# Optimization experiments

Measured on AMD Instinct MI355X. Metric: run time of the kernel, lower is better.

## Reference

```python
import jax, jax.numpy as jnp
import numpy as np

NUM_HEADS = 16


def setup_inputs() -> dict:
    key = jax.random.key(0)
    ks = jax.random.split(key, 8)
    B, S, E = 2, 2048, 1024
    std = 0.02
    return {
        "q": jax.random.normal(ks[0], (B, S, E), dtype=jnp.float32),
        "k": jax.random.normal(ks[1], (B, S, E), dtype=jnp.float32),
        "v": jax.random.normal(ks[2], (B, S, E), dtype=jnp.float32),
        "Wq": jax.random.normal(ks[3], (E, E), dtype=jnp.float32) * std,
        "Wk": jax.random.normal(ks[4], (E, E), dtype=jnp.float32) * std,
        "Wv": jax.random.normal(ks[5], (E, E), dtype=jnp.float32) * std,
        "Wo": jax.random.normal(ks[6], (E, E), dtype=jnp.float32) * std,
        "bo": jnp.zeros((E,), dtype=jnp.float32),
    }


def reference(q, k, v, Wq, Wk, Wv, Wo, bo):
    B, S, E = q.shape
    H = NUM_HEADS
    D = E // H
    # projections (nn.Linear: x @ W.T)
    Q = (q @ Wq.T).reshape(B, S, H, D).transpose(0, 2, 1, 3)  # [B,H,S,D]
    K = (k @ Wk.T).reshape(B, S, H, D).transpose(0, 2, 1, 3)
    V = (v @ Wv.T).reshape(B, S, H, D).transpose(0, 2, 1, 3)
    scores = jnp.einsum("bhsd,bhtd->bhst", Q, K)  # [B,H,S,S]
    # causal mask applied before scaling (as in source; -inf/sqrt(d) == -inf)
    causal = jnp.tril(jnp.ones((S, S), dtype=bool))
    scores = jnp.where(causal, scores, -jnp.inf)
    scores = scores / np.sqrt(D).astype(np.float32)
    attn = jax.nn.softmax(scores, axis=-1)
    out = jnp.einsum("bhst,bhtd->bhsd", attn, V)  # [B,H,S,D]
    out = out.transpose(0, 2, 1, 3).reshape(B, S, E)
    return out @ Wo.T + bo
```

## Files before the change

### kernel.cpp

```cpp
#include <hip/hip_runtime.h>

typedef unsigned short u16;
typedef __bf16 bf16x8 __attribute__((ext_vector_type(8)));
typedef float f32x4 __attribute__((ext_vector_type(4)));
typedef unsigned u32x4 __attribute__((ext_vector_type(4)));

#define B_ 2
#define S_ 2048
#define E_ 1024
#define H_ 16
#define D_ 64
#define M_ (B_ * S_)

__device__ inline u16 f2bf(float f) {
  union { float f; unsigned int u; } c; c.f = f;
  unsigned int u = c.u;
  return (u16)((u + 0x7FFFu + ((u >> 16) & 1u)) >> 16);
}

__device__ inline f32x4 mfma16(bf16x8 a, bf16x8 b, f32x4 c) {
  return __builtin_amdgcn_mfma_f32_16x16x32_bf16(a, b, c, 0, 0, 0);
}

__device__ inline void gload16(const void* g, void* lds) {
  __builtin_amdgcn_global_load_lds(
      (const __attribute__((address_space(1))) unsigned int*)g,
      (__attribute__((address_space(3))) unsigned int*)lds, 16, 0, 0);
}

struct CvtArgs {
  const float* src[4];
  u16* dst[4];
  int n[4];
};

__global__ __launch_bounds__(256) void cvt_kernel(CvtArgs a) {
  const int arr = blockIdx.y;
  const int n = a.n[arr];
  const float* __restrict__ s = a.src[arr];
  u16* __restrict__ d = a.dst[arr];
  const int stride = gridDim.x * blockDim.x;
  for (int i = blockIdx.x * blockDim.x + threadIdx.x; i * 4 < n; i += stride) {
    const float4 f = *(const float4*)(s + 4 * i);
    ushort4 o;
    o.x = f2bf(f.x); o.y = f2bf(f.y); o.z = f2bf(f.z); o.w = f2bf(f.w);
    *(ushort4*)(d + 4 * i) = o;
  }
}

__global__ __launch_bounds__(256, 3) void qkv_gemm(
    const float* __restrict__ qf, const float* __restrict__ kf,
    const float* __restrict__ vf, const u16* __restrict__ Wqb,
    const u16* __restrict__ Wkb, const u16* __restrict__ Wvb,
    u16* __restrict__ Qh, u16* __restrict__ Kh, u16* __restrict__ Vt) {
  constexpr int BM = 128, BN = 128, BK = 32;
  __shared__ alignas(16) u16 As[3][BM * BK];
  __shared__ alignas(16) u16 Bs[3][BN * BK];

  const int wg = blockIdx.x;
  const int xcd = wg & 7, idx = wg >> 3;
  const int nb = idx & 7, mz = idx >> 3;
  const int z = mz >> 2;
  const int m0 = (xcd * 4 + (mz & 3)) * BM, n0 = nb * BN;

  const float* A = (z == 0) ? qf  : (z == 1) ? kf  : vf;
  const u16* Bt  = (z == 0) ? Wqb : (z == 1) ? Wkb : Wvb;
  u16* outp      = (z == 0) ? Qh  : (z == 1) ? Kh  : Vt;

  const int tid = threadIdx.x;
  const int wave = tid >> 6, lane = tid & 63;
  const int wm = (wave >> 1) * 64, wn = (wave & 1) * 64;
  const int fr = lane & 15, fc = lane >> 4;
  const int lrow = lane >> 2;
  const int lcol_sw = (((lane & 3) ^ ((lrow >> 1) & 3)) * 8);

  const int arow_sub = lane >> 3;
  const int acol = (lane & 7) * 4;
  const int a_chunkbase = wave * 2;

  f32x4 acc[4][4] = {};

  u16 *aA = As[0], *aB = As[1], *aC = As[2];
  u16 *bA = Bs[0], *bB = Bs[1], *bC = Bs[2];

  float4 areg0[4], areg1[4];

  auto loadA0 = [&](int k0) {
#pragma unroll
    for (int ci = 0; ci < 2; ++ci)
#pragma unroll
      for (int i2 = 0; i2 < 2; ++i2) {
        const int row = (a_chunkbase + ci) * 16 + i2 * 8 + arow_sub;
        areg0[ci * 2 + i2] = *(const float4*)(A + (size_t)(m0 + row) * E_ + k0 + acol);
      }
  };
  auto loadA1 = [&](int k0) {
#pragma unroll
    for (int ci = 0; ci < 2; ++ci)
#pragma unroll
      for (int i2 = 0; i2 < 2; ++i2) {
        const int row = (a_chunkbase + ci) * 16 + i2 * 8 + arow_sub;
        areg1[ci * 2 + i2] = *(const float4*)(A + (size_t)(m0 + row) * E_ + k0 + acol);
      }
  };
  auto writeA0 = [&](u16* as) {
#pragma unroll
    for (int ci = 0; ci < 2; ++ci)
#pragma unroll
      for (int i2 = 0; i2 < 2; ++i2) {
        const int rowLoc = i2 * 8 + arow_sub;
        const int row = (a_chunkbase + ci) * 16 + rowLoc;
        const float4 f = areg0[ci * 2 + i2];
        unsigned d0, d1;
        asm("v_cvt_pk_bf16_f32 %0, %1, %2" : "=v"(d0) : "v"(f.x), "v"(f.y));
        asm("v_cvt_pk_bf16_f32 %0, %1, %2" : "=v"(d1) : "v"(f.z), "v"(f.w));
        const int slot = (acol >> 3) ^ ((rowLoc >> 1) & 3);
        const int half = (acol >> 2) & 1;
        *(uint2*)(&as[row * 32 + slot * 8 + half * 4]) = make_uint2(d0, d1);
      }
  };
  auto writeA1 = [&](u16* as) {
#pragma unroll
    for (int ci = 0; ci < 2; ++ci)
#pragma unroll
      for (int i2 = 0; i2 < 2; ++i2) {
        const int rowLoc = i2 * 8 + arow_sub;
        const int row = (a_chunkbase + ci) * 16 + rowLoc;
        const float4 f = areg1[ci * 2 + i2];
        unsigned d0, d1;
        asm("v_cvt_pk_bf16_f32 %0, %1, %2" : "=v"(d0) : "v"(f.x), "v"(f.y));
        asm("v_cvt_pk_bf16_f32 %0, %1, %2" : "=v"(d1) : "v"(f.z), "v"(f.w));
        const int slot = (acol >> 3) ^ ((rowLoc >> 1) & 3);
        const int half = (acol >> 2) & 1;
        *(uint2*)(&as[row * 32 + slot * 8 + half * 4]) = make_uint2(d0, d1);
      }
  };
  auto loadB = [&](int k0, u16* bs) {
#pragma unroll
    for (int i = 0; i < 2; ++i) {
      const int chunk = wave * 2 + i;
      const int row = chunk * 16 + lrow;
      gload16(Bt + (size_t)(n0 + row) * E_ + k0 + lcol_sw, bs + chunk * 16 * BK);
    }
  };

  const int sl = (fc ^ ((fr >> 1) & 3)) * 8;

  auto compute = [&]() {
    bf16x8 af[4], bfr[4];
#pragma unroll
    for (int mi = 0; mi < 4; ++mi)
      af[mi] = *(const bf16x8*)&aA[(wm + mi * 16 + fr) * BK + sl];
#pragma unroll
    for (int ni = 0; ni < 4; ++ni)
      bfr[ni] = *(const bf16x8*)&bA[(wn + ni * 16 + fr) * BK + sl];
    __builtin_amdgcn_s_setprio(1);
#pragma unroll
    for (int mi = 0; mi < 4; ++mi)
#pragma unroll
      for (int ni = 0; ni < 4; ++ni)
        acc[mi][ni] = mfma16(af[mi], bfr[ni], acc[mi][ni]);
    __builtin_amdgcn_s_setprio(0);
    u16* tp;
    tp = aA; aA = aB; aB = aC; aC = tp;
    tp = bA; bA = bB; bB = bC; bC = tp;
  };

  constexpr int NK = E_ / BK;
  loadA0(0);
  asm volatile("s_waitcnt vmcnt(0)" ::: "memory");
  writeA0(aA);
  loadA1(1 * BK);  loadB(0, bA);
  loadA0(2 * BK);  loadB(1 * BK, bB);

  for (int tt = 0; tt < NK; tt += 2) {
    {
      const int t = tt;
      if (t + 3 < NK) {
        asm volatile("s_waitcnt vmcnt(6)" ::: "memory");
      } else {
        asm volatile("s_waitcnt vmcnt(0)" ::: "memory");
      }
      asm volatile("s_waitcnt lgkmcnt(0)" ::: "memory");
      __builtin_amdgcn_s_barrier();
      __builtin_amdgcn_sched_barrier(0);
      writeA1(aB);
      if (t + 3 < NK) loadA1((t + 3) * BK);
      if (t + 2 < NK) loadB((t + 2) * BK, bC);
      __builtin_amdgcn_sched_barrier(0);
      compute();
    }
    {
      const int t = tt + 1;
      if (t + 1 < NK) {
        if (t + 3 < NK) {
          asm volatile("s_waitcnt vmcnt(6)" ::: "memory");
        } else {
          asm volatile("s_waitcnt vmcnt(0)" ::: "memory");
        }
      } else {
        asm volatile("s_waitcnt vmcnt(0)" ::: "memory");
      }
      asm volatile("s_waitcnt lgkmcnt(0)" ::: "memory");
      __builtin_amdgcn_s_barrier();
      __builtin_amdgcn_sched_barrier(0);
      if (t + 1 < NK) writeA0(aB);
      if (t + 3 < NK) loadA0((t + 3) * BK);
      if (t + 2 < NK) loadB((t + 2) * BK, bC);
      __builtin_amdgcn_sched_barrier(0);
      compute();
    }
  }

#pragma unroll
  for (int mi = 0; mi < 4; ++mi)
#pragma unroll
    for (int ni = 0; ni < 4; ++ni)
#pragma unroll
      for (int r = 0; r < 4; ++r) {
        const int m = m0 + wm + mi * 16 + (fc << 2) + r;
        const int n = n0 + wn + ni * 16 + fr;
        const float v = acc[mi][ni][r];
        const int b = m >> 11, s = m & (S_ - 1), h = n >> 6, d = n & 63;
        if (z != 2) {
          outp[((((size_t)b * H_ + h) * S_ + s) << 6) + d] = f2bf(v);
        } else {
          outp[(((size_t)b * H_ + h) * D_ + d) * S_ + s] = f2bf(v);
        }
      }
}

__global__ __launch_bounds__(256, 4) void oproj_gemm(
    const u16* __restrict__ A, const u16* __restrict__ Bt,
    const float* __restrict__ bias, float* __restrict__ outp) {
  constexpr int BM = 64, BN = 128, BK = 32;
  __shared__ alignas(16) u16 As[3][BM * BK];
  __shared__ alignas(16) u16 Bs[3][BN * BK];

  const int wg = blockIdx.x;
  const int xcd = wg & 7, idx = wg >> 3;
  const int nb = idx & 7, mi_ = idx >> 3;
  const int m0 = (xcd * 8 + mi_) * BM, n0 = nb * BN;

  const int tid = threadIdx.x;
  const int wave = tid >> 6, lane = tid & 63;
  const int wm = (wave >> 1) * 32, wn = (wave & 1) * 64;
  const int fr = lane & 15, fc = lane >> 4;
  const int lrow = lane >> 2;
  const int lcol_sw = (((lane & 3) ^ ((lrow >> 1) & 3)) * 8);

  f32x4 acc[2][4] = {};

  u16 *aA = As[0], *aB = As[1], *aC = As[2];
  u16 *bA = Bs[0], *bB = Bs[1], *bC = Bs[2];

  auto stage = [&](int k0, u16* as, u16* bs) {
#pragma unroll
    for (int i = 0; i < 3; ++i) {
      const int c = wave + 4 * i;
      if (c < 4)
        gload16(A + (size_t)(m0 + c * 16 + lrow) * E_ + k0 + lcol_sw, as + c * 16 * BK);
      else
        gload16(Bt + (size_t)(n0 + (c - 4) * 16 + lrow) * E_ + k0 + lcol_sw,
                bs + (c - 4) * 16 * BK);
    }
  };

  constexpr int NK = E_ / BK;
  stage(0, aA, bA);
  stage(BK, aB, bB);

  const int sl = (fc ^ ((fr >> 1) & 3)) * 8;

  for (int t = 0; t < NK; ++t) {
    if (t + 1 < NK) {
      asm volatile("s_waitcnt vmcnt(3)" ::: "memory");
    } else {
      asm volatile("s_waitcnt vmcnt(0)" ::: "memory");
    }
    __builtin_amdgcn_s_barrier();
    __builtin_amdgcn_sched_barrier(0);

    if (t + 2 < NK) stage((t + 2) * BK, aC, bC);

    bf16x8 af[2], bfr[4];
#pragma unroll
    for (int mi = 0; mi < 2; ++mi)
      af[mi] = *(const bf16x8*)&aA[(wm + mi * 16 + fr) * BK + sl];
#pragma unroll
    for (int ni = 0; ni < 4; ++ni)
      bfr[ni] = *(const bf16x8*)&bA[(wn + ni * 16 + fr) * BK + sl];
    __builtin_amdgcn_s_setprio(1);
#pragma unroll
    for (int mi = 0; mi < 2; ++mi)
#pragma unroll
      for (int ni = 0; ni < 4; ++ni)
        acc[mi][ni] = mfma16(af[mi], bfr[ni], acc[mi][ni]);
    __builtin_amdgcn_s_setprio(0);

    u16* tp;
    tp = aA; aA = aB; aB = aC; aC = tp;
    tp = bA; bA = bB; bB = bC; bC = tp;
  }

#pragma unroll
  for (int mi = 0; mi < 2; ++mi)
#pragma unroll
    for (int ni = 0; ni < 4; ++ni)
#pragma unroll
      for (int r = 0; r < 4; ++r) {
        const int m = m0 + wm + mi * 16 + (fc << 2) + r;
        const int n = n0 + wn + ni * 16 + fr;
        outp[(size_t)m * E_ + n] = acc[mi][ni][r] + bias[n];
      }
}


__device__ __forceinline__ void stage_kv128(
    const u16* __restrict__ Kh_head, const u16* __restrict__ Vt_head,
    int kv0, u16* kb, u16* vb, int wq, int lane) {
#pragma unroll
  for (int hh = 0; hh < 2; ++hh)
    gload16(Kh_head + (size_t)(kv0 + hh * 64 + lane) * D_ + wq * 8,
            kb + wq * 1024 + hh * 512);
#pragma unroll
  for (int i = 0; i < 2; ++i) {
    const int c = 2 * wq + i;
    gload16(Vt_head + (size_t)lane * S_ + kv0 + c * 8, vb + c * 512);
  }
}

__global__ __launch_bounds__(512, 4) void flash_attn(
    const u16* __restrict__ Qh, const u16* __restrict__ Kh,
    const u16* __restrict__ Vt, u16* __restrict__ O) {
  __shared__ alignas(16) u16 Kb[2][8192];
  __shared__ alignas(16) u16 Vb[2][8192];

  const int i = blockIdx.x;
  const int ch = i >> 8, p = i & 255;
  const int j = (ch << 8) + ((ch & 1) ? (255 - p) : p);
  const int qt = 15 - (j >> 5);
  const int bh = j & 31;

  const int tid = threadIdx.x;
  const int wq = tid >> 6, lane = tid & 63;

  const int q0 = qt * 128;
  const int b = bh >> 4, h = bh & 15;
  constexpr float SC = 0.125f * 1.4426950408889634f;
  const int fr = lane & 15, fc = lane >> 4;

  const u16* Qbase = Qh + ((size_t)bh * S_ + q0 + wq * 16 + fr) * D_ + 8 * fc;
  const bf16x8 qf0 = *(const bf16x8*)Qbase;
  const bf16x8 qf1 = *(const bf16x8*)(Qbase + 32);
  const u16* Kh_head = Kh + (size_t)bh * S_ * D_;
  const u16* Vt_head = Vt + (size_t)bh * D_ * S_;

  float lacc = 0.f;
  f32x4 oacc[4] = {};
  const int nt = qt + 1;

  u16 *kA = Kb[0], *kB = Kb[1];
  u16 *vA = Vb[0], *vB = Vb[1];

  stage_kv128(Kh_head, Vt_head, 0, kA, vA, wq, lane);

  for (int t = 0; t < nt; ++t) {
    asm volatile("s_waitcnt vmcnt(0)" ::: "memory");
    __builtin_amdgcn_s_barrier();
    __builtin_amdgcn_sched_barrier(0);

    if (t + 1 < nt)
      stage_kv128(Kh_head, Vt_head, (t + 1) * 128, kB, vB, wq, lane);

    const u16* kb = kA;
    const u16* vb = vA;
    const bool diag = (t == nt - 1);
    const int qg = q0 + wq * 16 + fr;

#pragma unroll
    for (int hh = 0; hh < 2; ++hh) {
      const int kvb = t * 128 + hh * 64;

      f32x4 sacc[4] = {};
      __builtin_amdgcn_s_setprio(1);
#pragma unroll
      for (int ni = 0; ni < 4; ++ni) {
        const bf16x8 k0 = *(const bf16x8*)&kb[fc * 1024 + hh * 512 + (16 * ni + fr) * 8];
        const bf16x8 k1 = *(const bf16x8*)&kb[(fc + 4) * 1024 + hh * 512 + (16 * ni + fr) * 8];
        sacc[ni] = mfma16(k0, qf0, sacc[ni]);
        sacc[ni] = mfma16(k1, qf1, sacc[ni]);
      }
      __builtin_amdgcn_s_setprio(0);

#pragma unroll
      for (int ni = 0; ni < 4; ++ni)
#pragma unroll
        for (int r = 0; r < 4; ++r) {
          const int kvg = kvb + 16 * ni + 4 * fc + r;
          float pv;
          if (diag && kvg > qg) {
            pv = 0.f;
          } else {
            pv = __builtin_amdgcn_exp2f(sacc[ni][r] * SC);
          }
          sacc[ni][r] = pv;
          lacc += pv;
        }

      unsigned w[4][2];
#pragma unroll
      for (int ni = 0; ni < 4; ++ni) {
        asm("v_cvt_pk_bf16_f32 %0, %1, %2"
            : "=v"(w[ni][0]) : "v"(sacc[ni][0]), "v"(sacc[ni][1]));
        asm("v_cvt_pk_bf16_f32 %0, %1, %2"
            : "=v"(w[ni][1]) : "v"(sacc[ni][2]), "v"(sacc[ni][3]));
      }

      unsigned paw0[4], paw1[4];
#pragma unroll
      for (int pair = 0; pair < 2; ++pair) {
        unsigned xx[2], yy[2], tt2[2];
#pragma unroll
        for (int hh2 = 0; hh2 < 2; ++hh2) {
          unsigned a = w[2 * pair][hh2], bb = w[2 * pair + 1][hh2];
          asm volatile("v_permlane32_swap_b32 %0, %1" : "+v"(a), "+v"(bb));
          xx[hh2] = a; yy[hh2] = bb;
          const unsigned s = (fc & 1) ? a : bb;
          tt2[hh2] = (unsigned)__shfl_xor((int)s, 16);
        }
        unsigned* pw_ = pair ? paw1 : paw0;
        pw_[0] = (fc & 1) ? tt2[0] : xx[0];
        pw_[1] = (fc & 1) ? tt2[1] : xx[1];
        pw_[2] = (fc & 1) ? yy[0] : tt2[0];
        pw_[3] = (fc & 1) ? yy[1] : tt2[1];
      }
      bf16x8 pa0, pa1;
      {
        u32x4 t0 = {paw0[0], paw0[1], paw0[2], paw0[3]};
        u32x4 t1 = {paw1[0], paw1[1], paw1[2], paw1[3]};
        __builtin_memcpy(&pa0, &t0, 16);
        __builtin_memcpy(&pa1, &t1, 16);
      }

      __builtin_amdgcn_s_setprio(1);
#pragma unroll
      for (int nd = 0; nd < 4; ++nd) {
        const bf16x8 v0 = *(const bf16x8*)&vb[(hh * 8 + fc) * 512 + (16 * nd + fr) * 8];
        const bf16x8 v1 = *(const bf16x8*)&vb[(hh * 8 + fc + 4) * 512 + (16 * nd + fr) * 8];
        oacc[nd] = mfma16(pa0, v0, oacc[nd]);
        oacc[nd] = mfma16(pa1, v1, oacc[nd]);
      }
      __builtin_amdgcn_s_setprio(0);
    }

    u16* tk = kA; kA = kB; kB = tk;
    u16* tv = vA; vA = vB; vB = tv;
  }

  float l = lacc;
  l += __shfl_xor(l, 16);
  l += __shfl_xor(l, 32);
  float linv[4];
#pragma unroll
  for (int r = 0; r < 4; ++r)
    linv[r] = __builtin_amdgcn_rcpf(__shfl(l, 4 * fc + r));

#pragma unroll
  for (int nd = 0; nd < 4; ++nd) {
#pragma unroll
    for (int r = 0; r < 4; ++r) {
      const int qr = q0 + wq * 16 + (fc << 2) + r;
      const int d = 16 * nd + fr;
      const float v = oacc[nd][r] * linv[r];
      O[((size_t)b * S_ + qr) * E_ + h * D_ + d] = f2bf(v);
    }
  }
}

extern "C" void kernel_launch(void* const* d_in, const int* in_sizes, int n_in,
                              void* d_out, int out_size, void* d_ws, size_t ws_size,
                              hipStream_t stream) {
  const float* q  = (const float*)d_in[0];
  const float* k  = (const float*)d_in[1];
  const float* v  = (const float*)d_in[2];
  const float* Wq = (const float*)d_in[3];
  const float* Wk = (const float*)d_in[4];
  const float* Wv = (const float*)d_in[5];
  const float* Wo = (const float*)d_in[6];
  const float* bo = (const float*)d_in[7];

  const size_t nBSE = (size_t)M_ * E_;
  const size_t nEE  = (size_t)E_ * E_;
  u16* Wqb = (u16*)d_ws;
  u16* Wkb = Wqb + nEE;
  u16* Wvb = Wkb + nEE;
  u16* Wob = Wvb + nEE;
  u16* Qh  = Wob + nEE;
  u16* Kh  = Qh + nBSE;
  u16* Vt  = Kh + nBSE;
  u16* Oa  = Vt + nBSE;

  CvtArgs ca;
  ca.src[0] = Wq; ca.dst[0] = Wqb; ca.n[0] = (int)nEE;
  ca.src[1] = Wk; ca.dst[1] = Wkb; ca.n[1] = (int)nEE;
  ca.src[2] = Wv; ca.dst[2] = Wvb; ca.n[2] = (int)nEE;
  ca.src[3] = Wo; ca.dst[3] = Wob; ca.n[3] = (int)nEE;
  cvt_kernel<<<dim3(256, 4), 256, 0, stream>>>(ca);

  qkv_gemm<<<dim3(768), 256, 0, stream>>>(
      q, k, v, Wqb, Wkb, Wvb, Qh, Kh, Vt);
  flash_attn<<<dim3(512), 512, 0, stream>>>(Qh, Kh, Vt, Oa);
  oproj_gemm<<<dim3(512), 256, 0, stream>>>(Oa, Wob, bo, (float*)d_out);
}
```

Before: 103.1 us.

## Switch QKV GEMM to double-buffered LDS pipeline and raise occupancy target

Replaces the triple-buffered LDS ring and the two alternating A-register stages in the QKV projection GEMM with a simpler double-buffered loop that keeps one A register set. The launch-bounds occupancy hint rises from 3 to 5 blocks per CU. Smaller LDS use and fewer registers are meant to let more workgroups hide latency. In exchange, each iteration now ends with a full vmcnt(0) wait and a barrier, so there is less prefetch depth and memory latency can become exposed.

```diff
diff --git a/kernel.cpp b/kernel.cpp
--- a/kernel.cpp
+++ b/kernel.cpp
@@ -48,14 +48,14 @@
   }
 }
 
-__global__ __launch_bounds__(256, 3) void qkv_gemm(
+__global__ __launch_bounds__(256, 5) void qkv_gemm(
     const float* __restrict__ qf, const float* __restrict__ kf,
     const float* __restrict__ vf, const u16* __restrict__ Wqb,
     const u16* __restrict__ Wkb, const u16* __restrict__ Wvb,
     u16* __restrict__ Qh, u16* __restrict__ Kh, u16* __restrict__ Vt) {
   constexpr int BM = 128, BN = 128, BK = 32;
-  __shared__ alignas(16) u16 As[3][BM * BK];
-  __shared__ alignas(16) u16 Bs[3][BN * BK];
+  __shared__ alignas(16) u16 As[2][BM * BK];
+  __shared__ alignas(16) u16 Bs[2][BN * BK];
 
   const int wg = blockIdx.x;
   const int xcd = wg & 7, idx = wg >> 3;
@@ -80,37 +80,28 @@
 
   f32x4 acc[4][4] = {};
 
-  u16 *aA = As[0], *aB = As[1], *aC = As[2];
-  u16 *bA = Bs[0], *bB = Bs[1], *bC = Bs[2];
-
-  float4 areg0[4], areg1[4];
-
-  auto loadA0 = [&](int k0) {
+  u16 *aA = As[0], *aB = As[1];
+  u16 *bA = Bs[0], *bB = Bs[1];
+
+  float4 areg[4];
+
+  auto loadA = [&](int k0) {
 #pragma unroll
     for (int ci = 0; ci < 2; ++ci)
 #pragma unroll
       for (int i2 = 0; i2 < 2; ++i2) {
         const int row = (a_chunkbase + ci) * 16 + i2 * 8 + arow_sub;
-        areg0[ci * 2 + i2] = *(const float4*)(A + (size_t)(m0 + row) * E_ + k0 + acol);
+        areg[ci * 2 + i2] = *(const float4*)(A + (size_t)(m0 + row) * E_ + k0 + acol);
       }
   };
-  auto loadA1 = [&](int k0) {
-#pragma unroll
-    for (int ci = 0; ci < 2; ++ci)
-#pragma unroll
-      for (int i2 = 0; i2 < 2; ++i2) {
-        const int row = (a_chunkbase + ci) * 16 + i2 * 8 + arow_sub;
-        areg1[ci * 2 + i2] = *(const float4*)(A + (size_t)(m0 + row) * E_ + k0 + acol);
-      }
-  };
-  auto writeA0 = [&](u16* as) {
+  auto writeA = [&](u16* as) {
 #pragma unroll
     for (int ci = 0; ci < 2; ++ci)
 #pragma unroll
       for (int i2 = 0; i2 < 2; ++i2) {
         const int rowLoc = i2 * 8 + arow_sub;
         const int row = (a_chunkbase + ci) * 16 + rowLoc;
-        const float4 f = areg0[ci * 2 + i2];
+        const float4 f = areg[ci * 2 + i2];
         unsigned d0, d1;
         asm("v_cvt_pk_bf16_f32 %0, %1, %2" : "=v"(d0) : "v"(f.x), "v"(f.y));
         asm("v_cvt_pk_bf16_f32 %0, %1, %2" : "=v"(d1) : "v"(f.z), "v"(f.w));
@@ -119,22 +110,6 @@
         *(uint2*)(&as[row * 32 + slot * 8 + half * 4]) = make_uint2(d0, d1);
       }
   };
-  auto writeA1 = [&](u16* as) {
-#pragma unroll
-    for (int ci = 0; ci < 2; ++ci)
-#pragma unroll
-      for (int i2 = 0; i2 < 2; ++i2) {
-        const int rowLoc = i2 * 8 + arow_sub;
-        const int row = (a_chunkbase + ci) * 16 + rowLoc;
-        const float4 f = areg1[ci * 2 + i2];
-        unsigned d0, d1;
-        asm("v_cvt_pk_bf16_f32 %0, %1, %2" : "=v"(d0) : "v"(f.x), "v"(f.y));
-        asm("v_cvt_pk_bf16_f32 %0, %1, %2" : "=v"(d1) : "v"(f.z), "v"(f.w));
-        const int slot = (acol >> 3) ^ ((rowLoc >> 1) & 3);
-        const int half = (acol >> 2) & 1;
-        *(uint2*)(&as[row * 32 + slot * 8 + half * 4]) = make_uint2(d0, d1);
-      }
-  };
   auto loadB = [&](int k0, u16* bs) {
 #pragma unroll
     for (int i = 0; i < 2; ++i) {
@@ -162,54 +137,31 @@
         acc[mi][ni] = mfma16(af[mi], bfr[ni], acc[mi][ni]);
     __builtin_amdgcn_s_setprio(0);
     u16* tp;
-    tp = aA; aA = aB; aB = aC; aC = tp;
-    tp = bA; bA = bB; bB = bC; bC = tp;
+    tp = aA; aA = aB; aB = tp;
+    tp = bA; bA = bB; bB = tp;
   };
 
   constexpr int NK = E_ / BK;
-  loadA0(0);
+  loadA(0);
   asm volatile("s_waitcnt vmcnt(0)" ::: "memory");
-  writeA0(aA);
-  loadA1(1 * BK);  loadB(0, bA);
-  loadA0(2 * BK);  loadB(1 * BK, bB);
-
-  for (int tt = 0; tt < NK; tt += 2) {
-    {
-      const int t = tt;
-      if (t + 3 < NK) {
-        asm volatile("s_waitcnt vmcnt(6)" ::: "memory");
-      } else {
-        asm volatile("s_waitcnt vmcnt(0)" ::: "memory");
-      }
-      asm volatile("s_waitcnt lgkmcnt(0)" ::: "memory");
-      __builtin_amdgcn_s_barrier();
-      __builtin_amdgcn_sched_barrier(0);
-      writeA1(aB);
-      if (t + 3 < NK) loadA1((t + 3) * BK);
-      if (t + 2 < NK) loadB((t + 2) * BK, bC);
-      __builtin_amdgcn_sched_barrier(0);
-      compute();
-    }
-    {
-      const int t = tt + 1;
-      if (t + 1 < NK) {
-        if (t + 3 < NK) {
-          asm volatile("s_waitcnt vmcnt(6)" ::: "memory");
-        } else {
-          asm volatile("s_waitcnt vmcnt(0)" ::: "memory");
-        }
-      } else {
-        asm volatile("s_waitcnt vmcnt(0)" ::: "memory");
-      }
-      asm volatile("s_waitcnt lgkmcnt(0)" ::: "memory");
-      __builtin_amdgcn_s_barrier();
-      __builtin_amdgcn_sched_barrier(0);
-      if (t + 1 < NK) writeA0(aB);
-      if (t + 3 < NK) loadA0((t + 3) * BK);
-      if (t + 2 < NK) loadB((t + 2) * BK, bC);
-      __builtin_amdgcn_sched_barrier(0);
-      compute();
-    }
+  writeA(aA);
+  loadB(0, bA);
+  loadA(1 * BK);
+  asm volatile("s_waitcnt vmcnt(0) lgkmcnt(0)" ::: "memory");
+  __builtin_amdgcn_s_barrier();
+
+  for (int t = 0; t < NK; ++t) {
+    if (t + 1 < NK) {
+      writeA(aB);
+      loadB((t + 1) * BK, bB);
+    }
+    if (t + 2 < NK) loadA((t + 2) * BK);
+    __builtin_amdgcn_sched_barrier(0);
+
+    compute();
+
+    asm volatile("s_waitcnt vmcnt(0) lgkmcnt(0)" ::: "memory");
+    __builtin_amdgcn_s_barrier();
   }
 
 #pragma unroll
@@ -314,7 +266,6 @@
         outp[(size_t)m * E_ + n] = acc[mi][ni][r] + bias[n];
       }
 }
-
 
 __device__ __forceinline__ void stage_kv128(
     const u16* __restrict__ Kh_head, const u16* __restrict__ Vt_head,
```

After: 283.2 us. 175% more time.
